# Performance work log

Measured on AMD Instinct MI355X. Metric: run time of the kernel, lower is better.

The kernel has to match this reference:

```python
import jax, jax.numpy as jnp
import numpy as np

N = 100000


def _gcn_conv(x, edge_index, W, b):
    # GCNConv with add_self_loops=True, symmetric normalization.
    src, dst = edge_index[0], edge_index[1]
    loop = jnp.arange(N, dtype=src.dtype)
    src = jnp.concatenate([src, loop])
    dst = jnp.concatenate([dst, loop])
    # degree of target nodes (edge weights all 1, incl. self loops)
    deg = jax.ops.segment_sum(jnp.ones_like(dst, dtype=x.dtype), dst, num_segments=N)
    dinv = jnp.where(deg > 0, jax.lax.rsqrt(deg), 0.0)
    norm = dinv[src] * dinv[dst]  # [E+N]
    h = x @ W  # [N, out]
    msg = h[src] * norm[:, None]  # gather + scale, [E+N, out]
    out = jax.ops.segment_sum(msg, dst, num_segments=N)  # scatter-add
    return out + b


def setup_inputs() -> dict:
    key = jax.random.key(0)
    k1, k2, k3, k4 = jax.random.split(key, 4)
    input_dim, hidden, output_dim = 256, 64, 128
    E = 1600000
    x = jax.random.normal(k1, (N, input_dim), dtype=jnp.float32)
    edge_index = jax.random.randint(k2, (2, E), 0, N, dtype=jnp.int64)
    W1 = jax.random.normal(k3, (input_dim, hidden), dtype=jnp.float32) / np.sqrt(input_dim)
    b1 = jnp.zeros((hidden,), dtype=jnp.float32)
    W2 = jax.random.normal(k4, (hidden, output_dim), dtype=jnp.float32) / np.sqrt(hidden)
    b2 = jnp.zeros((output_dim,), dtype=jnp.float32)
    return {"x": x, "edge_index": edge_index, "W1": W1, "b1": b1, "W2": W2, "b2": b2}


def reference(x, edge_index, W1, b1, W2, b2):
    h = jax.nn.relu(_gcn_conv(x, edge_index, W1, b1))
    return _gcn_conv(h, edge_index, W2, b2)
```

## Files before the change

### kernel.cpp

```cpp
#include <hip/hip_runtime.h>
#include <hip/hip_fp16.h>

#define NNODES 100000
#define NBUCK 391
#define NB_CHUNK 256
#define NC (NBUCK * NB_CHUNK)
#define SCAN_ELEMS 1024

typedef _Float16 f16x8 __attribute__((ext_vector_type(8)));
typedef float    f32x4 __attribute__((ext_vector_type(4)));

__global__ __launch_bounds__(256) void prep_kernel(const float* __restrict__ W1,
                                                   const float* __restrict__ W2,
                                                   const int* __restrict__ raw,
                                                   __half* __restrict__ wf1,
                                                   __half* __restrict__ wf2,
                                                   int* __restrict__ flag) {
    int b = blockIdx.x;
    if (b < 64) {
        int flat = b * 256 + threadIdx.x;
        int j  = flat & 7;
        int l  = (flat >> 3) & 63;
        int nb = (flat >> 9) & 3;
        int kc = flat >> 11;
        int k  = kc * 32 + ((l >> 4) << 3) + j;
        int nc = nb * 16 + (l & 15);
        wf1[flat] = __float2half(W1[k * 64 + nc]);
    } else if (b < 96) {
        int flat = (b - 64) * 256 + threadIdx.x;
        int j  = flat & 7;
        int l  = (flat >> 3) & 63;
        int nb = (flat >> 9) & 7;
        int kc = flat >> 12;
        int k  = kc * 32 + ((l >> 4) << 3) + j;
        int nc = nb * 16 + (l & 15);
        wf2[flat] = __float2half(W2[k * 128 + nc]);
    } else {
        __shared__ int cnt;
        if (threadIdx.x == 0) cnt = 0;
        __syncthreads();
        if (threadIdx.x < 100) {
            if (raw[2 * threadIdx.x + 1] == 0) atomicAdd(&cnt, 1);
        }
        __syncthreads();
        if (threadIdx.x == 0) *flag = (cnt > 50) ? 1 : 0;
    }
}

__global__ __launch_bounds__(256) void convert_gemm1_kernel(const int* __restrict__ raw,
                                                            int* __restrict__ src32,
                                                            int* __restrict__ dst32,
                                                            int* __restrict__ counts,
                                                            int E, int CE,
                                                            const int* __restrict__ flag,
                                                            const float* __restrict__ x,
                                                            const __half* __restrict__ wf,
                                                            __half* __restrict__ H, int M) {
    __shared__ __align__(16) char smem[64 * 264 * 2];
    int bid = blockIdx.x;
    if (bid < NB_CHUNK) {
        int* hist = (int*)smem;
        for (int i = threadIdx.x; i < NBUCK; i += 256) hist[i] = 0;
        __syncthreads();
        int isI64 = *flag;
        int beg = bid * CE;
        int end = beg + CE; if (end > E) end = E;
        const int2* raw2 = reinterpret_cast<const int2*>(raw);
        for (int e = beg + (int)threadIdx.x; e < end; e += 256) {
            int s, d;
            if (isI64) {
                s = raw2[e].x;
                d = raw2[E + e].x;
            } else {
                s = raw[e];
                d = raw[E + e];
            }
            src32[e] = s;
            dst32[e] = d;
            atomicAdd(&hist[d >> 8], 1);
        }
        __syncthreads();
        for (int k = threadIdx.x; k < NBUCK; k += 256)
            counts[k * NB_CHUNK + bid] = hist[k];
    } else {
        __half (*xs)[264] = (__half(*)[264])smem;
        int tid = threadIdx.x;
        int bm = (bid - NB_CHUNK) * 64;
        const float4* x4 = reinterpret_cast<const float4*>(x);
#pragma unroll
        for (int i = 0; i < 16; ++i) {
            int lin = i * 256 + tid;
            int row = lin >> 6;
            int c4  = lin & 63;
            int gr = bm + row; if (gr >= M) gr = M - 1;
            float4 v = x4[(size_t)gr * 64 + c4];
            __half* dst = &xs[row][c4 * 4];
            dst[0] = __float2half(v.x); dst[1] = __float2half(v.y);
            dst[2] = __float2half(v.z); dst[3] = __float2half(v.w);
        }
        __syncthreads();
        int w = tid >> 6;
        int l = tid & 63;
        int lrow = l & 15;
        int lk   = l >> 4;
        const f16x8* wf8 = reinterpret_cast<const f16x8*>(wf);
        f32x4 acc[4] = {};
#pragma unroll
        for (int kc = 0; kc < 8; ++kc) {
            f16x8 a = *reinterpret_cast<const f16x8*>(&xs[w * 16 + lrow][kc * 32 + lk * 8]);
#pragma unroll
            for (int nb = 0; nb < 4; ++nb) {
                f16x8 bfr = wf8[(kc * 4 + nb) * 64 + l];
                acc[nb] = __builtin_amdgcn_mfma_f32_16x16x32_f16(a, bfr, acc[nb], 0, 0, 0);
            }
        }
#pragma unroll
        for (int nb = 0; nb < 4; ++nb)
#pragma unroll
            for (int r = 0; r < 4; ++r) {
                int row = bm + w * 16 + lk * 4 + r;
                if (row < M) H[(size_t)row * 64 + nb * 16 + lrow] = __float2half(acc[nb][r]);
            }
    }
}

__global__ __launch_bounds__(256) void scan_partial_kernel(const int* __restrict__ in,
                                                           int* __restrict__ bsum, int n) {
    int base = blockIdx.x * SCAN_ELEMS + threadIdx.x * 4;
    int s = 0;
    if (base + 3 < n) {
        int4 v = *reinterpret_cast<const int4*>(&in[base]);
        s = v.x + v.y + v.z + v.w;
    } else {
        for (int i = base; i < n && i < base + 4; ++i) s += in[i];
    }
#pragma unroll
    for (int d = 32; d; d >>= 1) s += __shfl_down(s, d, 64);
    __shared__ int ws[4];
    int wid = threadIdx.x >> 6;
    if ((threadIdx.x & 63) == 0) ws[wid] = s;
    __syncthreads();
    if (threadIdx.x == 0) bsum[blockIdx.x] = ws[0] + ws[1] + ws[2] + ws[3];
}

__global__ void scan_partials_kernel(const int* __restrict__ bsum, int* __restrict__ boff,
                                     int* __restrict__ total_out, int nb) {
    __shared__ int s[128];
    int t = threadIdx.x;
    s[t] = (t < nb) ? bsum[t] : 0;
    __syncthreads();
    for (int d = 1; d < 128; d <<= 1) {
        int v = (t >= d) ? s[t - d] : 0;
        __syncthreads();
        s[t] += v;
        __syncthreads();
    }
    if (t < nb) boff[t] = (t == 0) ? 0 : s[t - 1];
    if (t == 127) *total_out = s[127];
}

__global__ __launch_bounds__(256) void scan_write_kernel(const int* __restrict__ in,
                                                         const int* __restrict__ boff,
                                                         int* __restrict__ outp, int n) {
    __shared__ int ts[256];
    int base = blockIdx.x * SCAN_ELEMS + threadIdx.x * 4;
    int v0 = 0, v1 = 0, v2 = 0, v3 = 0;
    if (base + 3 < n) {
        int4 v = *reinterpret_cast<const int4*>(&in[base]);
        v0 = v.x; v1 = v.y; v2 = v.z; v3 = v.w;
    } else {
        if (base < n)     v0 = in[base];
        if (base + 1 < n) v1 = in[base + 1];
        if (base + 2 < n) v2 = in[base + 2];
    }
    ts[threadIdx.x] = v0 + v1 + v2 + v3;
    __syncthreads();
    for (int d = 1; d < 256; d <<= 1) {
        int t = (threadIdx.x >= d) ? ts[threadIdx.x - d] : 0;
        __syncthreads();
        ts[threadIdx.x] += t;
        __syncthreads();
    }
    int run = boff[blockIdx.x] + ((threadIdx.x == 0) ? 0 : ts[threadIdx.x - 1]);
    if (base < n)     { outp[base] = run;     run += v0; }
    if (base + 1 < n) { outp[base + 1] = run; run += v1; }
    if (base + 2 < n) { outp[base + 2] = run; run += v2; }
    if (base + 3 < n) { outp[base + 3] = run; }
}

__global__ __launch_bounds__(256) void scatter_kernel(const int* __restrict__ src32,
                                                      const int* __restrict__ dst32,
                                                      const int* __restrict__ cbase,
                                                      int* __restrict__ cw,
                                                      int E, int CE) {
    __shared__ int cur[NBUCK];
    int b = blockIdx.x;
    for (int k = threadIdx.x; k < NBUCK; k += 256)
        cur[k] = cbase[k * NB_CHUNK + b];
    __syncthreads();
    int beg = b * CE;
    int end = beg + CE; if (end > E) end = E;
    for (int e = beg + (int)threadIdx.x; e < end; e += 256) {
        int s = src32[e];
        int d = dst32[e];
        int pos = atomicAdd(&cur[d >> 8], 1);
        cw[pos] = s | ((d & 255) << 24);
    }
}

__global__ __launch_bounds__(256) void bucketfin_kernel(const int* __restrict__ cw,
                                                        const int* __restrict__ cbase,
                                                        int* __restrict__ ptr,
                                                        float* __restrict__ dinv,
                                                        int* __restrict__ col,
                                                        int n, int E) {
    __shared__ int hist[256];
    __shared__ int sc[256];
    int tid = threadIdx.x;
    int k = blockIdx.x;
    hist[tid] = 0;
    __syncthreads();
    int beg = cbase[k * NB_CHUNK];
    int end = cbase[(k + 1) * NB_CHUNK];
    for (int e = beg + tid; e < end; e += 256)
        atomicAdd(&hist[(cw[e] >> 24) & 255], 1);
    __syncthreads();
    int dg = hist[tid];
    sc[tid] = dg;
    __syncthreads();
    for (int d = 1; d < 256; d <<= 1) {
        int t = (tid >= d) ? sc[tid - d] : 0;
        __syncthreads();
        sc[tid] += t;
        __syncthreads();
    }
    int p0 = beg + sc[tid] - dg;
    int i = (k << 8) + tid;
    if (i < n) {
        ptr[i] = p0;
        dinv[i] = rsqrtf((float)(dg + 1));
    }
    if (k == NBUCK - 1 && tid == 0) ptr[n] = E;
    __syncthreads();
    hist[tid] = p0;
    __syncthreads();
    for (int e = beg + tid; e < end; e += 256) {
        int v = cw[e];
        int pos = atomicAdd(&hist[(v >> 24) & 255], 1);
        col[pos] = v & 0x00FFFFFF;
    }
}

__global__ __launch_bounds__(256) void aggregate_kernel(const __half* __restrict__ h,
                                                        const int* __restrict__ ptr,
                                                        const int* __restrict__ col,
                                                        const float* __restrict__ dinv,
                                                        const float* __restrict__ bias,
                                                        __half* __restrict__ out, int n,
                                                        int relu) {
    int node = (blockIdx.x << 2) + (threadIdx.x >> 6);
    if (node >= n) return;
    int lane = threadIdx.x & 63;
    int g  = lane >> 3;
    int fl = (lane & 7) << 3;
    float acc[8] = {};
    int pend = ptr[node + 1];
    int p = ptr[node] + g;
    for (; p + 8 < pend; p += 16) {
        int c0 = col[p];
        int c1 = col[p + 8];
        uint4 r0 = *reinterpret_cast<const uint4*>(&h[(size_t)c0 * 64 + fl]);
        uint4 r1 = *reinterpret_cast<const uint4*>(&h[(size_t)c1 * 64 + fl]);
        float w0 = dinv[c0], w1 = dinv[c1];
        const unsigned* u0 = &r0.x;
        const unsigned* u1 = &r1.x;
#pragma unroll
        for (int k = 0; k < 4; ++k) {
            float2 f0 = __half22float2(*reinterpret_cast<const __half2*>(&u0[k]));
            float2 f1 = __half22float2(*reinterpret_cast<const __half2*>(&u1[k]));
            acc[2 * k]     = fmaf(w0, f0.x, acc[2 * k]);
            acc[2 * k + 1] = fmaf(w0, f0.y, acc[2 * k + 1]);
            acc[2 * k]     = fmaf(w1, f1.x, acc[2 * k]);
            acc[2 * k + 1] = fmaf(w1, f1.y, acc[2 * k + 1]);
        }
    }
    if (p < pend) {
        int c0 = col[p];
        uint4 r0 = *reinterpret_cast<const uint4*>(&h[(size_t)c0 * 64 + fl]);
        float w0 = dinv[c0];
        const unsigned* u0 = &r0.x;
#pragma unroll
        for (int k = 0; k < 4; ++k) {
            float2 f0 = __half22float2(*reinterpret_cast<const __half2*>(&u0[k]));
            acc[2 * k]     = fmaf(w0, f0.x, acc[2 * k]);
            acc[2 * k + 1] = fmaf(w0, f0.y, acc[2 * k + 1]);
        }
    }
#pragma unroll
    for (int j = 0; j < 8; ++j) {
        acc[j] += __shfl_xor(acc[j], 8, 64);
        acc[j] += __shfl_xor(acc[j], 16, 64);
        acc[j] += __shfl_xor(acc[j], 32, 64);
    }
    if (g == 0) {
        float di = dinv[node];
        uint4 sv = *reinterpret_cast<const uint4*>(&h[(size_t)node * 64 + fl]);
        const unsigned* su = &sv.x;
        float v[8];
#pragma unroll
        for (int k = 0; k < 4; ++k) {
            float2 f = __half22float2(*reinterpret_cast<const __half2*>(&su[k]));
            v[2 * k]     = fmaf(di, f.x, acc[2 * k]) * di;
            v[2 * k + 1] = fmaf(di, f.y, acc[2 * k + 1]) * di;
        }
        if (bias) {
            float4 b0 = *reinterpret_cast<const float4*>(&bias[fl]);
            float4 b1 = *reinterpret_cast<const float4*>(&bias[fl + 4]);
            v[0] += b0.x; v[1] += b0.y; v[2] += b0.z; v[3] += b0.w;
            v[4] += b1.x; v[5] += b1.y; v[6] += b1.z; v[7] += b1.w;
        }
        if (relu) {
#pragma unroll
            for (int j = 0; j < 8; ++j) v[j] = fmaxf(v[j], 0.f);
        }
        __half hv[8];
#pragma unroll
        for (int j = 0; j < 8; ++j) hv[j] = __float2half(v[j]);
        *reinterpret_cast<uint4*>(&out[(size_t)node * 64 + fl]) =
            *reinterpret_cast<const uint4*>(hv);
    }
}

__global__ __launch_bounds__(256) void gemm2_kernel(const __half* __restrict__ A,
                                                    const __half* __restrict__ wf,
                                                    const float* __restrict__ bias,
                                                    float* __restrict__ out, int M) {
    int tid = threadIdx.x;
    int w = tid >> 6;
    int l = tid & 63;
    int lrow = l & 15;
    int lk   = l >> 4;
    int base = blockIdx.x * 64 + w * 16;
    int arow = base + lrow; if (arow >= M) arow = M - 1;
    f16x8 a0 = *reinterpret_cast<const f16x8*>(&A[(size_t)arow * 64 + lk * 8]);
    f16x8 a1 = *reinterpret_cast<const f16x8*>(&A[(size_t)arow * 64 + 32 + lk * 8]);
    const f16x8* wf8 = reinterpret_cast<const f16x8*>(wf);
    f32x4 acc[8] = {};
#pragma unroll
    for (int nb = 0; nb < 8; ++nb) {
        acc[nb] = __builtin_amdgcn_mfma_f32_16x16x32_f16(a0, wf8[nb * 64 + l], acc[nb], 0, 0, 0);
        acc[nb] = __builtin_amdgcn_mfma_f32_16x16x32_f16(a1, wf8[(8 + nb) * 64 + l], acc[nb], 0, 0, 0);
    }
#pragma unroll
    for (int nb = 0; nb < 8; ++nb) {
        float bv = bias[nb * 16 + lrow];
#pragma unroll
        for (int r = 0; r < 4; ++r) {
            int row = base + lk * 4 + r;
            if (row < M) out[(size_t)row * 128 + nb * 16 + lrow] = acc[nb][r] + bv;
        }
    }
}

extern "C" void kernel_launch(void* const* d_in, const int* in_sizes, int n_in,
                              void* d_out, int out_size, void* d_ws, size_t ws_size,
                              hipStream_t stream) {
    const float* x  = (const float*)d_in[0];
    const int*   ei = (const int*)d_in[1];
    const float* W1 = (const float*)d_in[2];
    const float* b1 = (const float*)d_in[3];
    const float* W2 = (const float*)d_in[4];
    const float* b2 = (const float*)d_in[5];
    float* out = (float*)d_out;
    const int n = NNODES;
    const int E = in_sizes[1] / 2;
    const int CE = (E + NB_CHUNK - 1) / NB_CHUNK;

    char* w = (char*)d_ws;
    auto alloc = [&](size_t bytes) {
        char* p = w;
        w += (bytes + 255) & ~(size_t)255;
        return p;
    };
    int*    flag   = (int*)   alloc(4);
    int*    src32  = (int*)   alloc((size_t)E * 4);
    int*    dst32  = (int*)   alloc((size_t)E * 4);
    int*    counts = (int*)   alloc((size_t)NC * 4);
    int*    cbase  = (int*)   alloc((size_t)(NC + 1) * 4);
    float*  dinv   = (float*) alloc((size_t)n * 4);
    int*    ptr    = (int*)   alloc((size_t)(n + 1) * 4);
    int*    bsum   = (int*)   alloc(128 * 4);
    int*    boff   = (int*)   alloc(128 * 4);
    int*    cw     = (int*)   alloc((size_t)E * 4);
    int*    col    = (int*)   alloc((size_t)E * 4);
    __half* wfrag  = (__half*)alloc(16384 * 2);
    __half* wfrag2 = (__half*)alloc(8192 * 2);
    __half* H1     = (__half*)alloc((size_t)n * 64 * 2);
    __half* h1     = (__half*)alloc((size_t)n * 64 * 2);
    __half* A2     = (__half*)alloc((size_t)n * 64 * 2);

    int sbC = (NC + SCAN_ELEMS - 1) / SCAN_ELEMS;
    int g1b = (n + 63) / 64;

    prep_kernel<<<97, 256, 0, stream>>>(W1, W2, ei, wfrag, wfrag2, flag);
    convert_gemm1_kernel<<<NB_CHUNK + g1b, 256, 0, stream>>>(
        ei, src32, dst32, counts, E, CE, flag, x, wfrag, H1, n);
    scan_partial_kernel<<<sbC, 256, 0, stream>>>(counts, bsum, NC);
    scan_partials_kernel<<<1, 128, 0, stream>>>(bsum, boff, &cbase[NC], sbC);
    scan_write_kernel<<<sbC, 256, 0, stream>>>(counts, boff, cbase, NC);
    scatter_kernel<<<NB_CHUNK, 256, 0, stream>>>(src32, dst32, cbase, cw, E, CE);
    bucketfin_kernel<<<NBUCK, 256, 0, stream>>>(cw, cbase, ptr, dinv, col, n, E);

    aggregate_kernel<<<(n + 3) / 4, 256, 0, stream>>>(H1, ptr, col, dinv, b1, h1, n, 1);
    aggregate_kernel<<<(n + 3) / 4, 256, 0, stream>>>(h1, ptr, col, dinv, nullptr, A2, n, 0);
    gemm2_kernel<<<(n + 63) / 64, 256, 0, stream>>>(A2, wfrag2, b2, out, n);
}
```

Before: 178.1 us.

## Fuse three-pass bucket scan into one kernel via atomic block sums

The histogram pass now atomically accumulates per-1024-element block sums into bsum, which prep_kernel zeroes. The total is written in prep as E. The three scan kernels collapse into one scanw kernel, where every block redundantly scans the 128 block sums and then writes its own segment. This removes two kernel launches and a full pass over counts. Separately, it adds nontemporal loads for streamed edge/col arrays in scatter and aggregate, which may change cache behavior.

Result: slower. 462.9 us (+159.9%).

```diff
diff --git a/kernel.cpp b/kernel.cpp
--- a/kernel.cpp
+++ b/kernel.cpp
@@ -15,7 +15,9 @@
                                                    const int* __restrict__ raw,
                                                    __half* __restrict__ wf1,
                                                    __half* __restrict__ wf2,
-                                                   int* __restrict__ flag) {
+                                                   int* __restrict__ flag,
+                                                   int* __restrict__ bsum,
+                                                   int* __restrict__ cbase, int E) {
     int b = blockIdx.x;
     if (b < 64) {
         int flat = b * 256 + threadIdx.x;
@@ -38,6 +40,8 @@
     } else {
         __shared__ int cnt;
         if (threadIdx.x == 0) cnt = 0;
+        if (threadIdx.x < 128) bsum[threadIdx.x] = 0;
+        if (threadIdx.x == 128) cbase[NC] = E;
         __syncthreads();
         if (threadIdx.x < 100) {
             if (raw[2 * threadIdx.x + 1] == 0) atomicAdd(&cnt, 1);
@@ -51,6 +55,7 @@
                                                             int* __restrict__ src32,
                                                             int* __restrict__ dst32,
                                                             int* __restrict__ counts,
+                                                            int* __restrict__ bsum,
                                                             int E, int CE,
                                                             const int* __restrict__ flag,
                                                             const float* __restrict__ x,
@@ -80,8 +85,11 @@
             atomicAdd(&hist[d >> 8], 1);
         }
         __syncthreads();
-        for (int k = threadIdx.x; k < NBUCK; k += 256)
-            counts[k * NB_CHUNK + bid] = hist[k];
+        for (int k = threadIdx.x; k < NBUCK; k += 256) {
+            int hv = hist[k];
+            counts[k * NB_CHUNK + bid] = hv;
+            if (hv) atomicAdd(&bsum[k >> 2], hv);
+        }
     } else {
         __half (*xs)[264] = (__half(*)[264])smem;
         int tid = threadIdx.x;
@@ -124,68 +132,45 @@
     }
 }
 
-__global__ __launch_bounds__(256) void scan_partial_kernel(const int* __restrict__ in,
-                                                           int* __restrict__ bsum, int n) {
-    int base = blockIdx.x * SCAN_ELEMS + threadIdx.x * 4;
-    int s = 0;
-    if (base + 3 < n) {
-        int4 v = *reinterpret_cast<const int4*>(&in[base]);
-        s = v.x + v.y + v.z + v.w;
-    } else {
-        for (int i = base; i < n && i < base + 4; ++i) s += in[i];
-    }
-#pragma unroll
-    for (int d = 32; d; d >>= 1) s += __shfl_down(s, d, 64);
-    __shared__ int ws[4];
-    int wid = threadIdx.x >> 6;
-    if ((threadIdx.x & 63) == 0) ws[wid] = s;
-    __syncthreads();
-    if (threadIdx.x == 0) bsum[blockIdx.x] = ws[0] + ws[1] + ws[2] + ws[3];
-}
-
-__global__ void scan_partials_kernel(const int* __restrict__ bsum, int* __restrict__ boff,
-                                     int* __restrict__ total_out, int nb) {
-    __shared__ int s[128];
-    int t = threadIdx.x;
-    s[t] = (t < nb) ? bsum[t] : 0;
+__global__ __launch_bounds__(256) void scanw_kernel(const int* __restrict__ counts,
+                                                    const int* __restrict__ bsum,
+                                                    int* __restrict__ cbase, int n) {
+    __shared__ int ts[256];
+    __shared__ int bs[256];
+    int tid = threadIdx.x;
+    bs[tid] = (tid < 128) ? bsum[tid] : 0;
     __syncthreads();
     for (int d = 1; d < 128; d <<= 1) {
-        int v = (t >= d) ? s[t - d] : 0;
-        __syncthreads();
-        s[t] += v;
-        __syncthreads();
-    }
-    if (t < nb) boff[t] = (t == 0) ? 0 : s[t - 1];
-    if (t == 127) *total_out = s[127];
-}
-
-__global__ __launch_bounds__(256) void scan_write_kernel(const int* __restrict__ in,
-                                                         const int* __restrict__ boff,
-                                                         int* __restrict__ outp, int n) {
-    __shared__ int ts[256];
-    int base = blockIdx.x * SCAN_ELEMS + threadIdx.x * 4;
+        int v = (tid >= d) ? bs[tid - d] : 0;
+        __syncthreads();
+        bs[tid] += v;
+        __syncthreads();
+    }
+    int boff = (blockIdx.x == 0) ? 0 : bs[blockIdx.x - 1];
+
+    int base = blockIdx.x * SCAN_ELEMS + tid * 4;
     int v0 = 0, v1 = 0, v2 = 0, v3 = 0;
     if (base + 3 < n) {
-        int4 v = *reinterpret_cast<const int4*>(&in[base]);
+        int4 v = *reinterpret_cast<const int4*>(&counts[base]);
         v0 = v.x; v1 = v.y; v2 = v.z; v3 = v.w;
     } else {
-        if (base < n)     v0 = in[base];
-        if (base + 1 < n) v1 = in[base + 1];
-        if (base + 2 < n) v2 = in[base + 2];
-    }
-    ts[threadIdx.x] = v0 + v1 + v2 + v3;
+        if (base < n)     v0 = counts[base];
+        if (base + 1 < n) v1 = counts[base + 1];
+        if (base + 2 < n) v2 = counts[base + 2];
+    }
+    ts[tid] = v0 + v1 + v2 + v3;
     __syncthreads();
     for (int d = 1; d < 256; d <<= 1) {
-        int t = (threadIdx.x >= d) ? ts[threadIdx.x - d] : 0;
-        __syncthreads();
-        ts[threadIdx.x] += t;
-        __syncthreads();
-    }
-    int run = boff[blockIdx.x] + ((threadIdx.x == 0) ? 0 : ts[threadIdx.x - 1]);
-    if (base < n)     { outp[base] = run;     run += v0; }
-    if (base + 1 < n) { outp[base + 1] = run; run += v1; }
-    if (base + 2 < n) { outp[base + 2] = run; run += v2; }
-    if (base + 3 < n) { outp[base + 3] = run; }
+        int t = (tid >= d) ? ts[tid - d] : 0;
+        __syncthreads();
+        ts[tid] += t;
+        __syncthreads();
+    }
+    int run = boff + ((tid == 0) ? 0 : ts[tid - 1]);
+    if (base < n)     { cbase[base] = run;     run += v0; }
+    if (base + 1 < n) { cbase[base + 1] = run; run += v1; }
+    if (base + 2 < n) { cbase[base + 2] = run; run += v2; }
+    if (base + 3 < n) { cbase[base + 3] = run; }
 }
 
 __global__ __launch_bounds__(256) void scatter_kernel(const int* __restrict__ src32,
@@ -201,8 +186,8 @@
     int beg = b * CE;
     int end = beg + CE; if (end > E) end = E;
     for (int e = beg + (int)threadIdx.x; e < end; e += 256) {
-        int s = src32[e];
-        int d = dst32[e];
+        int s = __builtin_nontemporal_load(&src32[e]);
+        int d = __builtin_nontemporal_load(&dst32[e]);
         int pos = atomicAdd(&cur[d >> 8], 1);
         cw[pos] = s | ((d & 255) << 24);
     }
@@ -267,8 +252,8 @@
     int pend = ptr[node + 1];
     int p = ptr[node] + g;
     for (; p + 8 < pend; p += 16) {
-        int c0 = col[p];
-        int c1 = col[p + 8];
+        int c0 = __builtin_nontemporal_load(&col[p]);
+        int c1 = __builtin_nontemporal_load(&col[p + 8]);
         uint4 r0 = *reinterpret_cast<const uint4*>(&h[(size_t)c0 * 64 + fl]);
         uint4 r1 = *reinterpret_cast<const uint4*>(&h[(size_t)c1 * 64 + fl]);
         float w0 = dinv[c0], w1 = dinv[c1];
@@ -285,7 +270,7 @@
         }
     }
     if (p < pend) {
-        int c0 = col[p];
+        int c0 = __builtin_nontemporal_load(&col[p]);
         uint4 r0 = *reinterpret_cast<const uint4*>(&h[(size_t)c0 * 64 + fl]);
         float w0 = dinv[c0];
         const unsigned* u0 = &r0.x;
@@ -390,7 +375,6 @@
     float*  dinv   = (float*) alloc((size_t)n * 4);
     int*    ptr    = (int*)   alloc((size_t)(n + 1) * 4);
     int*    bsum   = (int*)   alloc(128 * 4);
-    int*    boff   = (int*)   alloc(128 * 4);
     int*    cw     = (int*)   alloc((size_t)E * 4);
     int*    col    = (int*)   alloc((size_t)E * 4);
     __half* wfrag  = (__half*)alloc(16384 * 2);
@@ -402,12 +386,10 @@
     int sbC = (NC + SCAN_ELEMS - 1) / SCAN_ELEMS;
     int g1b = (n + 63) / 64;
 
-    prep_kernel<<<97, 256, 0, stream>>>(W1, W2, ei, wfrag, wfrag2, flag);
+    prep_kernel<<<97, 256, 0, stream>>>(W1, W2, ei, wfrag, wfrag2, flag, bsum, cbase, E);
     convert_gemm1_kernel<<<NB_CHUNK + g1b, 256, 0, stream>>>(
-        ei, src32, dst32, counts, E, CE, flag, x, wfrag, H1, n);
-    scan_partial_kernel<<<sbC, 256, 0, stream>>>(counts, bsum, NC);
-    scan_partials_kernel<<<1, 128, 0, stream>>>(bsum, boff, &cbase[NC], sbC);
-    scan_write_kernel<<<sbC, 256, 0, stream>>>(counts, boff, cbase, NC);
+        ei, src32, dst32, counts, bsum, E, CE, flag, x, wfrag, H1, n);
+    scanw_kernel<<<sbC, 256, 0, stream>>>(counts, bsum, cbase, NC);
     scatter_kernel<<<NB_CHUNK, 256, 0, stream>>>(src32, dst32, cbase, cw, E, CE);
     bucketfin_kernel<<<NBUCK, 256, 0, stream>>>(cw, cbase, ptr, dinv, col, n, E);
 
```
